# Kernel optimization log

Measured on AMD Instinct MI355X. Metric: run time of the kernel, lower is better.

## Reference

```python
import jax, jax.numpy as jnp
import numpy as np

EPS = 1e-15

def gcn_sparse(x, row, col, ew, W, b, n):
    # PyG GCNConv: h = x@W; add self-loops (weight 1); sym-normalize; aggregate at col (target); + bias
    h = x @ W
    loop = jnp.arange(n)
    r = jnp.concatenate([row, loop])
    c = jnp.concatenate([col, loop])
    w = jnp.concatenate([ew, jnp.ones((n,), x.dtype)])
    deg = jax.ops.segment_sum(w, c, num_segments=n)
    dinv = jnp.where(deg > 0, deg ** -0.5, 0.0)
    norm = dinv[r] * w * dinv[c]
    out = jax.ops.segment_sum(norm[:, None] * h[r], c, num_segments=n)
    return out + b

def gcn_dense(x, adj, W, b):
    # Dense equivalent of dense_to_sparse + GCNConv: existing nonzero self-loops keep their
    # weight, zero-diagonal nodes get a self-loop of weight 1 (add_remaining_self_loops).
    diag = jnp.diagonal(adj)
    adj_h = adj + jnp.diag(jnp.where(diag == 0, 1.0, 0.0).astype(adj.dtype))
    deg = adj_h.sum(axis=0)  # degree at target (col) nodes
    dinv = jnp.where(deg > 0, deg ** -0.5, 0.0)
    a_norm = dinv[:, None] * adj_h * dinv[None, :]  # norm_ij = d_i^-1/2 a_ij d_j^-1/2
    return a_norm.T @ (x @ W) + b  # out_j = sum_i norm_ij h_i

def diff_pool(x, adj, s, mask=None):
    s = jax.nn.softmax(s, axis=-1)
    if mask is not None:
        x = x * mask[:, None]
        s = s * mask[:, None]
    out = s.T @ x                      # [C, F]
    out_adj = s.T @ (adj @ s)          # [C, C]
    link = jnp.linalg.norm(adj - s @ s.T) / adj.size
    ent = jnp.mean(jnp.sum(-s * jnp.log(s + EPS), axis=-1))
    return out, out_adj, link, ent

def setup_inputs() -> dict:
    N, E, F, H, C1, C2, NC = 8192, 262144, 128, 128, 1024, 128, 16
    key = jax.random.key(0)
    ks = jax.random.split(key, 16)
    x0 = jax.random.normal(ks[0], (N, F), dtype=jnp.float32)
    edge_index = jax.random.randint(ks[1], (2, E), 0, N, dtype=jnp.int32)
    edge_weight = jax.random.uniform(ks[2], (E,), dtype=jnp.float32)
    adj = jnp.zeros((N, N), jnp.float32).at[edge_index[0], edge_index[1]].add(edge_weight)
    mask = jnp.ones((N,), jnp.float32)
    g = lambda k, i, o: jax.random.normal(k, (i, o), dtype=jnp.float32) * (1.0 / np.sqrt(i))
    return {
        'x0': x0, 'edge_index': edge_index, 'edge_weight': edge_weight,
        'adj': adj, 'mask': mask,
        'W0_in': g(ks[3], F, H),      'b0_in': jnp.zeros((H,)),
        'Wp1':   g(ks[4], H, C1),     'bp1':   jnp.zeros((C1,)),
        'W1_in': g(ks[5], H, H),      'b1_in': jnp.zeros((H,)),
        'Wp2':   g(ks[6], H, C2),     'bp2':   jnp.zeros((C2,)),
        'W2_in': g(ks[7], H, H),      'b2_in': jnp.zeros((H,)),
        'W1_out': g(ks[8], 2 * H, H), 'b1_out': jnp.zeros((H,)),
        'W0_out': g(ks[9], 2 * H, NC), 'b0_out': jnp.zeros((NC,)),
    }

def reference(x0, edge_index, edge_weight, adj, mask,
              W0_in, b0_in, Wp1, bp1, W1_in, b1_in, Wp2, bp2,
              W2_in, b2_in, W1_out, b1_out, W0_out, b0_out):
    n = x0.shape[0]
    row, col = edge_index[0], edge_index[1]
    x0_ = jax.nn.relu(gcn_sparse(x0, row, col, edge_weight, W0_in, b0_in, n))
    s1 = jax.nn.relu(gcn_sparse(x0_, row, col, edge_weight, Wp1, bp1, n))
    x1, adj1, l1, e1 = diff_pool(x0_, adj, s1, mask)
    x1_ = jax.nn.relu(gcn_dense(x1, adj1, W1_in, b1_in))
    s2 = jax.nn.relu(gcn_dense(x1_, adj1, Wp2, bp2))
    x2, adj2, l2, e2 = diff_pool(x1_, adj1, s2)
    x2_out = jax.nn.relu(gcn_dense(x2, adj2, W2_in, b2_in))
    x2_out_up = s2 @ x2_out  # unpool with pre-softmax relu s2, as in source
    x1_out = jax.nn.relu(gcn_dense(jnp.concatenate([x1_, x2_out_up], axis=1), adj1, W1_out, b1_out))
    x1_out_up = s1 @ x1_out
    x0_out = jax.nn.relu(gcn_sparse(jnp.concatenate([x0_, x1_out_up], axis=1), row, col, edge_weight, W0_out, b0_out, n))
    prediction = jax.nn.log_softmax(x0_out, axis=1)
    edge_loss = l1 + e1 + l2 + e2
    return prediction, s1, edge_loss, adj1
```

## Files before the change

### kernel.cpp

```cpp
#include <hip/hip_runtime.h>
#include <math.h>


#define N_NODES 8192
#define N_EDGES 262144

typedef __attribute__((ext_vector_type(8))) short short8;
typedef __attribute__((ext_vector_type(4))) float floatx4;

#define OFF_DEG     0
#define OFF_CNTC    8192
#define OFF_CNTR    16384
#define OFF_SCAL    24576
#define ZERO_FLOATS 24592
#define OFF_COLPTR  24592
#define OFF_ROWPTR  32785
#define OFF_CURC    40978
#define OFF_CURR    49170
#define OFF_COLR    57362
#define OFF_COLN    319506
#define OFF_ROWC    581650
#define OFF_ROWW    843794
#define OFF_DINV    1105938
#define OFF_X0      1114144
#define OFF_H0      2162720
#define OFF_S       3211296
#define OFF_AN1TB   OFF_S
#define OFF_ADJ1B   (OFF_S+524288)
#define OFF_HAT     (OFF_S+1048576)
#define OFF_HBT     (OFF_S+1114112)
#define OFF_HCATT   (OFF_S+1179648)
#define OFF_S2ST    (OFF_S+1245184)
#define OFF_X0T     7405600
#define OFF_X0B     7929888
#define A2          8454176
#define OFF_X1      (A2+0)
#define OFF_Y16     (A2+131072)
#define OFF_X1_     (A2+262144)
#define OFF_S2      (A2+524288)
#define OFF_S2S     (A2+655360)
#define OFF_U       (A2+786432)
#define OFF_X2      (A2+917504)
#define OFF_ADJ2    (A2+933888)
#define OFF_HC      (A2+950272)
#define OFF_X2_     (A2+966656)
#define OFF_AN2     (A2+983040)
#define OFF_Z2      (A2+999424)
#define OFF_HCAT    (A2+1130496)
#define OFF_X1O     (A2+1261568)
#define OFF_P16     (A2+1392640)
#define OFF_DI1     (A2+1654784)
#define OFF_DF1     (A2+1655808)
#define OFF_DI2     (A2+1656832)
#define OFF_DF2     (A2+1656960)
#define OFF_ST      10111264
#define OFF_TBF     14305568
#define OFF_WP1T    OFF_TBF
#define OFF_PADJ    OFF_TBF
#define OFF_PG      22694176
#define OFF_PP      OFF_PG
#define OFF_PX1     31082784
#define OFF_TT2     32131360

#define OUT_PRED 0
#define OUT_S1   131072
#define OUT_LOSS 8519680
#define OUT_ADJ1 8519681

__device__ __forceinline__ unsigned short f2bf(float f) {
    union { float f; unsigned u; } v; v.f = f;
    unsigned r = (v.u + 0x7FFF + ((v.u >> 16) & 1)) >> 16;
    return (unsigned short)r;
}
__device__ __forceinline__ float bf2f(unsigned short b) {
    union { unsigned u; float f; } v; v.u = (unsigned)b << 16; return v.f;
}


__global__ void k_hist(const int* __restrict__ row, const int* __restrict__ col,
                       const float* __restrict__ ew, int E,
                       float* deg, int* cntc, int* cntr, float* sumA2) {
    __shared__ float red[256];
    int e = blockIdx.x * 256 + threadIdx.x;
    float w2 = 0.f;
    if (e < E) {
        int r = row[e], c = col[e];
        float w = ew[e];
        atomicAdd(&deg[c], w);
        atomicAdd(&cntc[c], 1);
        atomicAdd(&cntr[r], 1);
        w2 = w * w;
    }
    red[threadIdx.x] = w2; __syncthreads();
    for (int s = 128; s > 0; s >>= 1) { if (threadIdx.x < s) red[threadIdx.x] += red[threadIdx.x + s]; __syncthreads(); }
    if (threadIdx.x == 0) atomicAdd(sumA2, red[0]);
}

__global__ __launch_bounds__(1024) void k_scan(const int* cntc, const int* cntr,
        int* colptr, int* rowptr, int* curc, int* curr, int n, int E,
        const float* __restrict__ deg, float* __restrict__ dinv) {
    __shared__ int part[1024];
    int tid = threadIdx.x;
    const int per = 8;
    for (int pass = 0; pass < 2; ++pass) {
        const int* cnt = pass ? cntr : cntc;
        int* ptr = pass ? rowptr : colptr;
        int* cur = pass ? curr : curc;
        int st = tid * per;
// ... 117 lines not shown
    for (int k0 = 0; k0 < K; k0 += 32) {
        #pragma unroll
        for (int l = 0; l < 4; ++l) {
            int idx = tid + 256 * l;
            int r = idx >> 5, c = idx & 31;
            As[r][c] = A[(size_t)(m0 + r) * K + k0 + c];
            Bs[r][c] = B[(size_t)(k0 + r) * N + n0 + c];
        }
        __syncthreads();
        #pragma unroll
        for (int kk = 0; kk < 32; ++kk) {
            float a0 = As[ty * 2][kk], a1 = As[ty * 2 + 1][kk];
            float b0 = Bs[kk][tx * 2], b1 = Bs[kk][tx * 2 + 1];
            acc[0][0] += a0 * b0; acc[0][1] += a0 * b1;
            acc[1][0] += a1 * b0; acc[1][1] += a1 * b1;
        }
        __syncthreads();
    }
    #pragma unroll
    for (int i = 0; i < 2; ++i)
        #pragma unroll
        for (int j = 0; j < 2; ++j)
            As[ty * 2 + i][tx * 2 + j] = acc[i][j];
    __syncthreads();
    int nl = tid >> 3, moff = (tid & 7) * 4;
    ushort4 o;
    o.x = f2bf(As[moff + 0][nl]);
    o.y = f2bf(As[moff + 1][nl]);
    o.z = f2bf(As[moff + 2][nl]);
    o.w = f2bf(As[moff + 3][nl]);
    *(ushort4*)(CT + (size_t)(n0 + nl) * M + m0 + moff) = o;
}

__global__ __launch_bounds__(256) void gemm_atb32(const float* __restrict__ A, const float* __restrict__ B,
        float* __restrict__ C, int M, int N, int K,
        const float* __restrict__ bias, int relu, float* sumsq_acc) {
    __shared__ float As[32][33];
    __shared__ float Bs[32][33];
    __shared__ float red[256];
    int tid = threadIdx.x, tx = tid & 15, ty = tid >> 4;
    int m0 = blockIdx.y * 32, n0 = blockIdx.x * 32;
    float acc[2][2] = {};
    for (int k0 = 0; k0 < K; k0 += 32) {
        #pragma unroll
        for (int l = 0; l < 4; ++l) {
            int idx = tid + 256 * l;
            int r = idx >> 5, c = idx & 31;
            As[c][r] = A[(size_t)(k0 + r) * M + m0 + c];
            Bs[r][c] = B[(size_t)(k0 + r) * N + n0 + c];
        }
        __syncthreads();
        #pragma unroll
        for (int kk = 0; kk < 32; ++kk) {
            float a0 = As[ty * 2][kk], a1 = As[ty * 2 + 1][kk];
            float b0 = Bs[kk][tx * 2], b1 = Bs[kk][tx * 2 + 1];
            acc[0][0] += a0 * b0; acc[0][1] += a0 * b1;
            acc[1][0] += a1 * b0; acc[1][1] += a1 * b1;
        }
        __syncthreads();
    }
    if (sumsq_acc) {
        float ss = acc[0][0] * acc[0][0] + acc[0][1] * acc[0][1]
                 + acc[1][0] * acc[1][0] + acc[1][1] * acc[1][1];
        red[tid] = ss; __syncthreads();
        for (int s = 128; s > 0; s >>= 1) { if (tid < s) red[tid] += red[tid + s]; __syncthreads(); }
        if (tid == 0) atomicAdd(sumsq_acc, red[0]);
        return;
    }
    #pragma unroll
    for (int i = 0; i < 2; ++i)
        #pragma unroll
        for (int j = 0; j < 2; ++j) {
            int m = m0 + ty * 2 + i, n = n0 + tx * 2 + j;
            float v = acc[i][j];
            if (bias) v += bias[n];
            if (relu) v = fmaxf(v, 0.f);
            C[(size_t)m * N + n] = v;
        }
}

__global__ __launch_bounds__(256) void k_atb32_3(const float* __restrict__ A,
        const float* __restrict__ B0, const float* __restrict__ B1, const float* __restrict__ B2,
        float* __restrict__ C0, float* __restrict__ C1, float* ss_acc,
        int M, int N, int K) {
    __shared__ float As[32][33];
    __shared__ float Bs[32][33];
    __shared__ float red[256];
    int op = blockIdx.z;
    const float* B = (op == 0) ? B0 : (op == 1) ? B1 : B2;
    int tid = threadIdx.x, tx = tid & 15, ty = tid >> 4;
    int m0 = blockIdx.y * 32, n0 = blockIdx.x * 32;
    float acc[2][2] = {};
    for (int k0 = 0; k0 < K; k0 += 32) {
        #pragma unroll
        for (int l = 0; l < 4; ++l) {
            int idx = tid + 256 * l;
            int r = idx >> 5, c = idx & 31;
            As[c][r] = A[(size_t)(k0 + r) * M + m0 + c];
            Bs[r][c] = B[(size_t)(k0 + r) * N + n0 + c];
        }
        __syncthreads();
        #pragma unroll
        for (int kk = 0; kk < 32; ++kk) {
            float a0 = As[ty * 2][kk], a1 = As[ty * 2 + 1][kk];
            float b0 = Bs[kk][tx * 2], b1 = Bs[kk][tx * 2 + 1];
            acc[0][0] += a0 * b0; acc[0][1] += a0 * b1;
            acc[1][0] += a1 * b0; acc[1][1] += a1 * b1;
        }
        __syncthreads();
    }
// ... 10 lines not shown
    for (int i = 0; i < 2; ++i)
        #pragma unroll
        for (int j = 0; j < 2; ++j)
            C[(size_t)(m0 + ty * 2 + i) * N + n0 + tx * 2 + j] = acc[i][j];
}

__global__ __launch_bounds__(256) void k_gemm_n16(const float* __restrict__ A, const float* __restrict__ B,
        float* __restrict__ C, int M, int K, int accum) {
    __shared__ float As[16][64];
    __shared__ float Bs[64][16];
    int tid = threadIdx.x;
    int r = tid >> 4, c = tid & 15;
    int m0 = blockIdx.x * 16;
    float acc = 0.f;
    for (int k0 = 0; k0 < K; k0 += 64) {
        #pragma unroll
        for (int l = 0; l < 4; ++l) {
            int idx = tid + 256 * l;
            int rr = idx >> 6, cc = idx & 63;
            As[rr][cc] = A[(size_t)(m0 + rr) * K + k0 + cc];
            int kk = idx >> 4, c2 = idx & 15;
            Bs[kk][c2] = B[(size_t)(k0 + kk) * 16 + c2];
        }
        __syncthreads();
        #pragma unroll 16
        for (int kk = 0; kk < 64; ++kk) acc += As[r][kk] * Bs[kk][c];
        __syncthreads();
    }
    float* p = &C[(size_t)(m0 + r) * 16 + c];
    if (accum) acc += *p;
    *p = acc;
}


__global__ __launch_bounds__(256) void gemm_tn_bf16_part(
        const unsigned short* __restrict__ A, const unsigned short* __restrict__ B,
        float* __restrict__ P, int M, int N, int K) {
    __shared__ __align__(16) unsigned short As[128 * 64];
    __shared__ __align__(16) unsigned short Bs[128 * 64];
    int tid = threadIdx.x;
    int wave = tid >> 6, lane = tid & 63;
    int wm = wave >> 1, wn = wave & 1;
    int m0 = blockIdx.x * 128, n0 = blockIdx.y * 128;
    int kchunk = K / gridDim.z;
    int k0 = blockIdx.z * kchunk;
    float* Pz = P + (size_t)blockIdx.z * M * N;
    floatx4 acc[4][4] = {};
    int sr = tid >> 3;
    int sc = (tid & 7) * 8;
    int q = lane >> 4, lm = lane & 15;
    for (int kt = 0; kt < kchunk; kt += 64) {
        #pragma unroll
        for (int p = 0; p < 4; ++p) {
            int mrow = sr + p * 32;
            int gk = k0 + kt + sc;
            int scs = sc ^ ((mrow & 7) * 8);
            *(short8*)(&As[mrow * 64 + scs]) = *(const short8*)(&A[(size_t)(m0 + mrow) * K + gk]);
            *(short8*)(&Bs[mrow * 64 + scs]) = *(const short8*)(&B[(size_t)(n0 + mrow) * K + gk]);
        }
        __syncthreads();
        #pragma unroll
        for (int ks = 0; ks < 64; ks += 32) {
            short8 af[4], bf[4];
            int kk = ks + q * 8;
            #pragma unroll
            for (int i = 0; i < 4; ++i) {
                int ml = wm * 64 + i * 16 + lm;
                af[i] = *(const short8*)(&As[ml * 64 + (kk ^ ((ml & 7) * 8))]);
                int nl = wn * 64 + i * 16 + lm;
                bf[i] = *(const short8*)(&Bs[nl * 64 + (kk ^ ((nl & 7) * 8))]);
            }
            #pragma unroll
            for (int i = 0; i < 4; ++i)
                #pragma unroll
                for (int j = 0; j < 4; ++j)
                    acc[i][j] = __builtin_amdgcn_mfma_f32_16x16x32_bf16(af[i], bf[j], acc[i][j], 0, 0, 0);
        }
        __syncthreads();
    }
    for (int i = 0; i < 4; ++i) {
        int rowb = m0 + wm * 64 + i * 16 + q * 4;
        for (int j = 0; j < 4; ++j) {
            int col = n0 + wn * 64 + j * 16 + lm;
            #pragma unroll
            for (int r = 0; r < 4; ++r)
                Pz[(size_t)(rowb + r) * N + col] = acc[i][j][r];
        }
    }
}

__global__ __launch_bounds__(256) void gemm_tn_bf16_part3(
        const unsigned short* __restrict__ A,
        const unsigned short* __restrict__ B0, const unsigned short* __restrict__ B1,
        const unsigned short* __restrict__ B2,
        float* __restrict__ P0, float* __restrict__ P1, float* __restrict__ P2,
        int K) {
    __shared__ __align__(16) unsigned short As[128 * 64];
    __shared__ __align__(16) unsigned short Bs[128 * 64];
    int tid = threadIdx.x;
    int wave = tid >> 6, lane = tid & 63;
    int wm = wave >> 1, wn = wave & 1;
    int by = blockIdx.y;
    const unsigned short* B; float* P; int N, n0;
    if (by < 8)       { B = B0; P = P0; N = 1024; n0 = by * 128; }
    else if (by < 16) { B = B1; P = P1; N = 1024; n0 = (by - 8) * 128; }
    else              { B = B2; P = P2; N = 128;  n0 = 0; }
    int m0 = blockIdx.x * 128;
    int kchunk = K / gridDim.z;
    int k0 = blockIdx.z * kchunk;
    float* Pz = P + (size_t)blockIdx.z * 1024 * N;
    floatx4 acc[4][4] = {};
    int sr = tid >> 3;
    int sc = (tid & 7) * 8;
    int q = lane >> 4, lm = lane & 15;
    for (int kt = 0; kt < kchunk; kt += 64) {
        #pragma unroll
        for (int p = 0; p < 4; ++p) {
            int mrow = sr + p * 32;
            int gk = k0 + kt + sc;
            int scs = sc ^ ((mrow & 7) * 8);
            *(short8*)(&As[mrow * 64 + scs]) = *(const short8*)(&A[(size_t)(m0 + mrow) * K + gk]);
            *(short8*)(&Bs[mrow * 64 + scs]) = *(const short8*)(&B[(size_t)(n0 + mrow) * K + gk]);
        }
        __syncthreads();
        #pragma unroll
        for (int ks = 0; ks < 64; ks += 32) {
            short8 af[4], bf[4];
            int kk = ks + q * 8;
            #pragma unroll
            for (int i = 0; i < 4; ++i) {
                int ml = wm * 64 + i * 16 + lm;
                af[i] = *(const short8*)(&As[ml * 64 + (kk ^ ((ml & 7) * 8))]);
                int nl = wn * 64 + i * 16 + lm;
                bf[i] = *(const short8*)(&Bs[nl * 64 + (kk ^ ((nl & 7) * 8))]);
            }
            #pragma unroll
            for (int i = 0; i < 4; ++i)
                #pragma unroll
                for (int j = 0; j < 4; ++j)
                    acc[i][j] = __builtin_amdgcn_mfma_f32_16x16x32_bf16(af[i], bf[j], acc[i][j], 0, 0, 0);
        }
        __syncthreads();
    }
    for (int i = 0; i < 4; ++i) {
        int rowb = m0 + wm * 64 + i * 16 + q * 4;
        for (int j = 0; j < 4; ++j) {
            int col = n0 + wn * 64 + j * 16 + lm;
            #pragma unroll
            for (int r = 0; r < 4; ++r)
                Pz[(size_t)(rowb + r) * N + col] = acc[i][j][r];
        }
    }
}

__global__ __launch_bounds__(256) void gemm_tn_bf16_store(
        const unsigned short* __restrict__ A, const unsigned short* __restrict__ B,
        float* __restrict__ C, int M, int N, int K,
        const float* __restrict__ bias, int relu) {
    __shared__ __align__(16) unsigned short As[128 * 64];
    __shared__ __align__(16) unsigned short Bs[128 * 64];
    int tid = threadIdx.x;
    int wave = tid >> 6, lane = tid & 63;
    int wm = wave >> 1, wn = wave & 1;
    int m0 = blockIdx.x * 128, n0 = blockIdx.y * 128;
    floatx4 acc[4][4] = {};
    int sr = tid >> 3;
    int sc = (tid & 7) * 8;
    int q = lane >> 4, lm = lane & 15;
    for (int kt = 0; kt < K; kt += 64) {
        #pragma unroll
        for (int p = 0; p < 4; ++p) {
            int mrow = sr + p * 32;
            int gk = kt + sc;
            int scs = sc ^ ((mrow & 7) * 8);
            *(short8*)(&As[mrow * 64 + scs]) = *(const short8*)(&A[(size_t)(m0 + mrow) * K + gk]);
            *(short8*)(&Bs[mrow * 64 + scs]) = *(const short8*)(&B[(size_t)(n0 + mrow) * K + gk]);
        }
        __syncthreads();
        #pragma unroll
        for (int ks = 0; ks < 64; ks += 32) {
            short8 af[4], bf[4];
            int kk = ks + q * 8;
            #pragma unroll
            for (int i = 0; i < 4; ++i) {
                int ml = wm * 64 + i * 16 + lm;
                af[i] = *(const short8*)(&As[ml * 64 + (kk ^ ((ml & 7) * 8))]);
                int nl = wn * 64 + i * 16 + lm;
                bf[i] = *(const short8*)(&Bs[nl * 64 + (kk ^ ((nl & 7) * 8))]);
            }
            #pragma unroll
            for (int i = 0; i < 4; ++i)
                #pragma unroll
                for (int j = 0; j < 4; ++j)
                    acc[i][j] = __builtin_amdgcn_mfma_f32_16x16x32_bf16(af[i], bf[j], acc[i][j], 0, 0, 0);
        }
        __syncthreads();
    }
    for (int i = 0; i < 4; ++i) {
        int rowb = m0 + wm * 64 + i * 16 + q * 4;
        for (int j = 0; j < 4; ++j) {
            int col = n0 + wn * 64 + j * 16 + lm;
            float bv = bias ? bias[col] : 0.f;
            #pragma unroll
            for (int r = 0; r < 4; ++r) {
                float v = acc[i][j][r] + bv;
                if (relu) v = fmaxf(v, 0.f);
                C[(size_t)(rowb + r) * N + col] = v;
            }
        }
    }
}

__global__ __launch_bounds__(256) void k_reduce4(const float* __restrict__ P,
        float* __restrict__ C, unsigned short* __restrict__ Cb,
        int n, int nsplit, float* ss_acc) {
    __shared__ float red[256];
    float ss = 0.f;
    for (int i4 = (blockIdx.x * 256 + threadIdx.x) * 4; i4 < n; i4 += gridDim.x * 256 * 4) {
        float4 v = *(const float4*)(P + i4);
        for (int s = 1; s < nsplit; ++s) {
            float4 w = *(const float4*)(P + (size_t)s * n + i4);
            v.x += w.x; v.y += w.y; v.z += w.z; v.w += w.w;
        }
        if (C) *(float4*)(C + i4) = v;
        if (Cb) {
            ushort4 o; o.x = f2bf(v.x); o.y = f2bf(v.y); o.z = f2bf(v.z); o.w = f2bf(v.w);
            *(ushort4*)(Cb + i4) = o;
        }
        ss += v.x * v.x + v.y * v.y + v.z * v.z + v.w * v.w;
    }
    if (!ss_acc) return;
    red[threadIdx.x] = ss; __syncthreads();
    for (int s = 128; s > 0; s >>= 1) { if (threadIdx.x < s) red[threadIdx.x] += red[threadIdx.x + s]; __syncthreads(); }
    if (threadIdx.x == 0) atomicAdd(ss_acc, red[0]);
}

__global__ __launch_bounds__(256) void k_reduce_br(const float* __restrict__ P,
        float* __restrict__ C, int n, int N, int nsplit,
        const float* __restrict__ bias, int relu) {
    for (int i4 = (blockIdx.x * 256 + threadIdx.x) * 4; i4 < n; i4 += gridDim.x * 256 * 4) {
        float4 v = *(const float4*)(P + i4);
        for (int s = 1; s < nsplit; ++s) {
            float4 w = *(const float4*)(P + (size_t)s * n + i4);
            v.x += w.x; v.y += w.y; v.z += w.z; v.w += w.w;
        }
        if (bias) {
            float4 b = *(const float4*)(bias + (i4 % N));
            v.x += b.x; v.y += b.y; v.z += b.z; v.w += b.w;
        }
        if (relu) {
            v.x = fmaxf(v.x, 0.f); v.y = fmaxf(v.y, 0.f);
            v.z = fmaxf(v.z, 0.f); v.w = fmaxf(v.w, 0.f);
        }
        *(float4*)(C + i4) = v;
    }
}


__global__ __launch_bounds__(256) void k_transpose_f2b(
        const float* __restrict__ in, unsigned short* __restrict__ outb,
        int R, int C, const float* __restrict__ rowscale) {
    __shared__ float tile[64][65];
    int rb = blockIdx.y * 64, cb = blockIdx.x * 64;
    int t = threadIdx.x;
    int lr = t >> 4, lc4 = (t & 15) * 4;
    #pragma unroll
    for (int p = 0; p < 4; ++p) {
// ... 179 lines not shown
__global__ __launch_bounds__(256) void k_softmax_ent(const float* __restrict__ x, float* __restrict__ S,
        int W, const float* __restrict__ mask, float* ent_acc) {
    __shared__ float red[256];
    int row = blockIdx.x, tid = threadIdx.x;
    const float* xr = x + (size_t)row * W;
    float m = -3.0e38f;
    for (int q = tid; q < W; q += 256) m = fmaxf(m, xr[q]);
    red[tid] = m; __syncthreads();
    for (int s = 128; s > 0; s >>= 1) { if (tid < s) red[tid] = fmaxf(red[tid], red[tid + s]); __syncthreads(); }
    m = red[0]; __syncthreads();
    float sum = 0.f;
    for (int q = tid; q < W; q += 256) sum += expf(xr[q] - m);
    red[tid] = sum; __syncthreads();
    for (int s = 128; s > 0; s >>= 1) { if (tid < s) red[tid] += red[tid + s]; __syncthreads(); }
    float inv = 1.0f / red[0]; __syncthreads();
    float mk = mask ? mask[row] : 1.0f;
    float* Sr = S + (size_t)row * W;
    float ent = 0.f;
    for (int q = tid; q < W; q += 256) {
        float v = expf(xr[q] - m) * inv * mk;
        Sr[q] = v;
        ent -= v * logf(v + 1e-15f);
    }
    red[tid] = ent; __syncthreads();
    for (int s = 128; s > 0; s >>= 1) { if (tid < s) red[tid] += red[tid + s]; __syncthreads(); }
    if (tid == 0) atomicAdd(ent_acc, red[0]);
}

__global__ __launch_bounds__(256) void k_spmm_seg(const unsigned short* __restrict__ Sb,
        const int* __restrict__ rptr, const int* __restrict__ rowc, const float* __restrict__ roww,
        unsigned short* __restrict__ tb) {
    int wave = threadIdx.x >> 6, lane = threadIdx.x & 63;
    int r = blockIdx.x * 4 + wave;
    int j0 = blockIdx.y * 128 + lane * 2;
    const unsigned short* Sj = Sb + j0;
    float a0 = 0.f, a1 = 0.f;
    int e0 = rptr[r], e1 = rptr[r + 1];
    int e = e0;
    for (; e + 4 <= e1; e += 4) {
        int c0 = rowc[e], c1 = rowc[e + 1], c2 = rowc[e + 2], c3 = rowc[e + 3];
        float w0 = roww[e], w1 = roww[e + 1], w2 = roww[e + 2], w3 = roww[e + 3];
        unsigned v0 = *(const unsigned*)(Sj + (size_t)c0 * 1024);
        unsigned v1 = *(const unsigned*)(Sj + (size_t)c1 * 1024);
        unsigned v2 = *(const unsigned*)(Sj + (size_t)c2 * 1024);
        unsigned v3 = *(const unsigned*)(Sj + (size_t)c3 * 1024);
        a0 += w0 * bf2f((unsigned short)(v0 & 0xffff)) + w1 * bf2f((unsigned short)(v1 & 0xffff))
            + w2 * bf2f((unsigned short)(v2 & 0xffff)) + w3 * bf2f((unsigned short)(v3 & 0xffff));
        a1 += w0 * bf2f((unsigned short)(v0 >> 16)) + w1 * bf2f((unsigned short)(v1 >> 16))
            + w2 * bf2f((unsigned short)(v2 >> 16)) + w3 * bf2f((unsigned short)(v3 >> 16));
    }
    for (; e < e1; ++e) {
        int c = rowc[e]; float w = roww[e];
        unsigned v = *(const unsigned*)(Sj + (size_t)c * 1024);
        a0 += w * bf2f((unsigned short)(v & 0xffff));
        a1 += w * bf2f((unsigned short)(v >> 16));
    }
    unsigned o = (unsigned)f2bf(a0) | ((unsigned)f2bf(a1) << 16);
    *(unsigned*)(tb + (size_t)r * 1024 + j0) = o;
}

__global__ void k_colsum_part(const float* __restrict__ adjm, int n, float* part) {
    int j = blockIdx.x * blockDim.x + threadIdx.x;
    if (j >= n) return;
    int r0 = blockIdx.y * 64;
    float s = 0.f;
    for (int r = r0; r < r0 + 64; ++r) s += adjm[(size_t)r * n + j];
    part[(size_t)blockIdx.y * n + j] = s;
}

__global__ void k_dfix_part(const float* __restrict__ adjm, int n, const float* __restrict__ part,
                            int nparts, float* dinvv, float* dfix, float* cross_acc) {
    __shared__ float red[256];
    int j = blockIdx.x * blockDim.x + threadIdx.x;
    float diag = 0.f;
    if (j < n) {
        float s = 0.f;
        for (int p = 0; p < nparts; ++p) s += part[(size_t)p * n + j];
        diag = adjm[(size_t)j * n + j];
        float fix = (diag == 0.f) ? 1.0f : 0.f;
        s += fix;
        dfix[j] = fix;
        dinvv[j] = (s > 0.f) ? 1.0f / sqrtf(s) : 0.f;
    }
    red[threadIdx.x] = diag; __syncthreads();
    for (int s = 128; s > 0; s >>= 1) { if (threadIdx.x < s) red[threadIdx.x] += red[threadIdx.x + s]; __syncthreads(); }
    if (threadIdx.x == 0) atomicAdd(cross_acc, red[0]);
}

__global__ __launch_bounds__(128) void k_coldfix128(const float* __restrict__ adjm,
        float* dinvv, float* dfix, float* cross2_out) {
    __shared__ float red[128];
    int j = threadIdx.x;
    float s = 0.f;
    for (int i = 0; i < 128; ++i) s += adjm[(size_t)i * 128 + j];
    float diag = adjm[(size_t)j * 128 + j];
    float fix = (diag == 0.f) ? 1.0f : 0.f;
    s += fix;
    dfix[j] = fix;
    dinvv[j] = (s > 0.f) ? 1.0f / sqrtf(s) : 0.f;
    red[j] = diag; __syncthreads();
    for (int st = 64; st > 0; st >>= 1) { if (j < st) red[j] += red[j + st]; __syncthreads(); }
    if (j == 0) *cross2_out = red[0];
}

__global__ void k_anorm(const float* __restrict__ adjm, int n, const float* __restrict__ dinvv,
                        const float* __restrict__ dfix, float* __restrict__ anorm) {
    int idx = blockIdx.x * 256 + threadIdx.x;
    if (idx >= n * n) return;
    int i = idx / n, j = idx % n;
    float v = adjm[idx] + ((i == j) ? dfix[j] : 0.f);
    anorm[idx] = dinvv[i] * v * dinvv[j];
}

__global__ void k_finalize(const float* __restrict__ sc, float* loss) {
    if (threadIdx.x == 0 && blockIdx.x == 0) {
        float e1     = sc[0] / 8192.0f;
        float cross  = sc[1];
        float g2     = sc[2];
        float sumA2  = sc[3];
        float ssadj1 = sc[4];
        float e2     = sc[5] / 1024.0f;
        float cross2 = sc[6];
        float g2b    = sc[7];
        float l1 = sqrtf(fmaxf(sumA2 - 2.0f * cross + g2, 0.f)) / 67108864.0f;
        float l2 = sqrtf(fmaxf(ssadj1 - 2.0f * cross2 + g2b, 0.f)) / 1048576.0f;
        *loss = l1 + e1 + l2 + e2;
    }
}


extern "C" void kernel_launch(void* const* d_in, const int* in_sizes, int n_in,
                              void* d_out, int out_size, void* d_ws, size_t ws_size,
                              hipStream_t stream) {
    const int N = N_NODES, E = N_EDGES;
    const float* x0     = (const float*)d_in[0];
    const int*   eidx   = (const int*)d_in[1];
    const float* ew     = (const float*)d_in[2];
    const float* mask   = (const float*)d_in[4];
    const float* W0_in  = (const float*)d_in[5];
    const float* b0_in  = (const float*)d_in[6];
    const float* Wp1    = (const float*)d_in[7];
    const float* bp1    = (const float*)d_in[8];
    const float* W1_in  = (const float*)d_in[9];
    const float* b1_in  = (const float*)d_in[10];
// ... 26 lines not shown
    float* coln  = wsf + OFF_COLN;
    int*   rowc  = wsi + OFF_ROWC;
    float* roww  = wsf + OFF_ROWW;
    float* dinv  = wsf + OFF_DINV;
    float* x0_   = wsf + OFF_X0;
    unsigned short* h0b   = (unsigned short*)(wsf + OFF_H0);
    unsigned short* Sb    = (unsigned short*)(wsf + OFF_S);
    unsigned short* TT    = (unsigned short*)(wsf + OFF_TT2);
    unsigned short* AN1TB = (unsigned short*)(wsf + OFF_AN1TB);
    unsigned short* ADJ1B = (unsigned short*)(wsf + OFF_ADJ1B);
    unsigned short* HAT   = (unsigned short*)(wsf + OFF_HAT);
    unsigned short* HBT   = (unsigned short*)(wsf + OFF_HBT);
    unsigned short* HCATT = (unsigned short*)(wsf + OFF_HCATT);
    unsigned short* S2ST  = (unsigned short*)(wsf + OFF_S2ST);
    unsigned short* ST    = (unsigned short*)(wsf + OFF_ST);
    unsigned short* TBF   = (unsigned short*)(wsf + OFF_TBF);
    unsigned short* WP1T  = (unsigned short*)(wsf + OFF_WP1T);
    unsigned short* X0T   = (unsigned short*)(wsf + OFF_X0T);
    unsigned short* x0b   = (unsigned short*)(wsf + OFF_X0B);
    float* PADJ  = wsf + OFF_PADJ;
    float* PG    = wsf + OFF_PG;
    float* PP    = wsf + OFF_PP;
    float* PX1   = wsf + OFF_PX1;
    float* x1    = wsf + OFF_X1;
    float* y16   = wsf + OFF_Y16;
    float* x1_   = wsf + OFF_X1_;
    float* s2    = wsf + OFF_S2;
    float* S2s   = wsf + OFF_S2S;
    float* u     = wsf + OFF_U;
    float* x2    = wsf + OFF_X2;
    float* adj2  = wsf + OFF_ADJ2;
    float* hC    = wsf + OFF_HC;
    float* x2_   = wsf + OFF_X2_;
    float* an2   = wsf + OFF_AN2;
    float* z2    = wsf + OFF_Z2;
    float* hcat  = wsf + OFF_HCAT;
    float* x1o_  = wsf + OFF_X1O;
    float* p16   = wsf + OFF_P16;
    float* di1   = wsf + OFF_DI1;
    float* df1   = wsf + OFF_DF1;
    float* di2   = wsf + OFF_DI2;
    float* df2   = wsf + OFF_DF2;
    float* cspart = wsf + OFF_CURC;

    const int* row = eidx;
    const int* col = eidx + E;

    hipMemsetAsync(wsf, 0, (size_t)ZERO_FLOATS * sizeof(float), stream);

    k_hist<<<E / 256, 256, 0, stream>>>(row, col, ew, E, deg, cntc, cntr, &scal[3]);
    k_scan<<<1, 1024, 0, stream>>>(cntc, cntr, cptr, rptr, curc, curr, N, E, deg, dinv);
    k_scatter<<<E / 256, 256, 0, stream>>>(row, col, ew, E, dinv, curc, curr, colr, coln, rowc, roww);

    gemm_ab_b16<<<dim3(2, 128), 256, 0, stream>>>(x0, W0_in, h0b, 8192, 128, 128);
    k_agg_b16<<<N, 64, 0, stream>>>(h0b, x0_, x0b, cptr, colr, coln, dinv, b0_in, 1);

    k_agg_b16<<<N, 64, 0, stream>>>(x0b, nullptr, h0b, cptr, colr, coln, dinv, nullptr, 0);
    k_transpose_f2b<<<dim3(16, 2), 256, 0, stream>>>(Wp1, WP1T, 128, 1024, nullptr);
    gemm_tn_bf16_store<<<dim3(64, 8), 256, 0, stream>>>(h0b, WP1T, s1o, 8192, 1024, 128, bp1, 1);

    k_softmax1024<<<N, 256, 0, stream>>>(s1o, Sb, mask, &scal[0]);
    k_spmm_seg<<<dim3(N / 4, 8), 256, 0, stream>>>(Sb, rptr, rowc, roww, TBF);
    k_transpose_b2b2<<<dim3(16, 128, 2), 256, 0, stream>>>(Sb, ST, TBF, TT, 8192, 1024);
    k_transpose_f2b<<<dim3(2, 128), 256, 0, stream>>>(x0_, X0T, 8192, 128, mask);

    gemm_tn_bf16_part3<<<dim3(8, 17, 8), 256, 0, stream>>>(ST, TT, ST, X0T, PADJ, PG, PX1, 8192);
    k_reduce4<<<1024, 256, 0, stream>>>(PADJ, adj1o, ADJ1B, 1024 * 1024, 8, &scal[4]);
    k_reduce4<<<1024, 256, 0, stream>>>(PG, nullptr, nullptr, 1024 * 1024, 8, &scal[2]);
    k_reduce4<<<128, 256, 0, stream>>>(PX1, x1, nullptr, 1024 * 128, 8, nullptr);

    k_colsum_part<<<dim3(4, 16), 256, 0, stream>>>(adj1o, 1024, cspart);
    k_dfix_part<<<4, 256, 0, stream>>>(adj1o, 1024, cspart, 16, di1, df1, &scal[1]);
    k_anorm_tb<<<dim3(16, 16), 256, 0, stream>>>(adj1o, 1024, di1, df1, AN1TB);

    gemm_ab32_bt<<<dim3(4, 32), 256, 0, stream>>>(x1, W1_in, HAT, 1024, 128, 128);
    gemm_tn_bf16_part<<<dim3(8, 1, 16), 256, 0, stream>>>(AN1TB, HAT, PP, 1024, 128, 1024);
    k_reduce_br<<<128, 256, 0, stream>>>(PP, x1_, 1024 * 128, 128, 16, b1_in, 1);
    gemm_ab32_bt<<<dim3(4, 32), 256, 0, stream>>>(x1_, Wp2, HBT, 1024, 128, 128);
    gemm_tn_bf16_part<<<dim3(8, 1, 16), 256, 0, stream>>>(AN1TB, HBT, PP, 1024, 128, 1024);
    k_reduce_br<<<128, 256, 0, stream>>>(PP, s2, 1024 * 128, 128, 16, bp2, 1);

    k_softmax_ent<<<1024, 256, 0, stream>>>(s2, S2s, 128, nullptr, &scal[5]);
    k_transpose_f2b<<<dim3(2, 16), 256, 0, stream>>>(S2s, S2ST, 1024, 128, nullptr);
    gemm_tn_bf16_part<<<dim3(8, 1, 16), 256, 0, stream>>>(ADJ1B, S2ST, PP, 1024, 128, 1024);
    k_reduce_br<<<128, 256, 0, stream>>>(PP, u, 1024 * 128, 128, 16, nullptr, 0);
    k_atb32_3<<<dim3(4, 4, 3), 256, 0, stream>>>(S2s, x1_, u, S2s, x2, adj2, &scal[7], 128, 128, 1024);

    k_coldfix128<<<1, 128, 0, stream>>>(adj2, di2, df2, &scal[6]);
    k_anorm<<<64, 256, 0, stream>>>(adj2, 128, di2, df2, an2);
    gemm_ab32<<<dim3(4, 4), 256, 0, stream>>>(x2, W2_in, hC, 128, 128, 128, nullptr, 0, 0);
    gemm_atb32<<<dim3(4, 4), 256, 0, stream>>>(an2, hC, x2_, 128, 128, 128, b2_in, 1, nullptr);

    gemm_ab32<<<dim3(4, 4), 256, 0, stream>>>(x2_, W1_out + 128 * 128, z2, 128, 128, 128, nullptr, 0, 0);
    gemm_ab32<<<dim3(4, 32), 256, 0, stream>>>(x1_, W1_out, hcat, 1024, 128, 128, nullptr, 0, 0);
    gemm_ab32<<<dim3(4, 32), 256, 0, stream>>>(s2, z2, hcat, 1024, 128, 128, nullptr, 0, 1);
    k_transpose_f2b<<<dim3(2, 16), 256, 0, stream>>>(hcat, HCATT, 1024, 128, nullptr);
    gemm_tn_bf16_part<<<dim3(8, 1, 16), 256, 0, stream>>>(AN1TB, HCATT, PP, 1024, 128, 1024);
    k_reduce_br<<<128, 256, 0, stream>>>(PP, x1o_, 1024 * 128, 128, 16, b1_out, 1);

    k_gemm_n16<<<64, 256, 0, stream>>>(x1o_, W0_out + 128 * 16, y16, 1024, 128, 0);
    k_gemm_n16<<<512, 256, 0, stream>>>(x0_, W0_out, p16, 8192, 128, 0);
    k_gemm_n16<<<512, 256, 0, stream>>>(s1o, y16, p16, 8192, 1024, 1);
    k_agg16_ls<<<512, 256, 0, stream>>>(p16, predo, cptr, colr, coln, dinv, b0_out);

    k_finalize<<<1, 64, 0, stream>>>(scal, losso);
}
```

Measured before the change: 967.4 us.

## Fuse small kernels, use direct global-to-LDS loads in bf16 GEMMs, widen spmm

Several launch pairs are merged into single kernels: the three partial-sum reductions, the column-sum and degree-fix passes, the normalized-adjacency build folded into the 128x128 GEMM, the two-source concat GEMMs plus transpose, and the two n16 GEMMs. The bf16 MFMA GEMMs now stage tiles with global_load_lds instead of going through registers. The segment spmm processes four columns per lane instead of two. The aim is fewer launches and intermediate buffers and cheaper tile staging, at the cost of more complex kernels and reliance on the swizzle staying correct under the new LDS write pattern.

```diff
diff --git a/kernel.cpp b/kernel.cpp
--- a/kernel.cpp
+++ b/kernel.cpp
@@ -44,9 +44,7 @@
 #define OFF_ADJ2    (A2+933888)
 #define OFF_HC      (A2+950272)
 #define OFF_X2_     (A2+966656)
-#define OFF_AN2     (A2+983040)
 #define OFF_Z2      (A2+999424)
-#define OFF_HCAT    (A2+1130496)
 #define OFF_X1O     (A2+1261568)
 #define OFF_P16     (A2+1392640)
 #define OFF_DI1     (A2+1654784)
@@ -74,6 +72,11 @@
 }
 __device__ __forceinline__ float bf2f(unsigned short b) {
     union { unsigned u; float f; } v; v.u = (unsigned)b << 16; return v.f;
+}
+__device__ __forceinline__ void gl_lds16(const unsigned short* g, unsigned short* l) {
+    __builtin_amdgcn_global_load_lds(
+        (const __attribute__((address_space(1))) void*)g,
+        (__attribute__((address_space(3))) void*)l, 16, 0, 0);
 }
 
 
@@ -257,12 +260,57 @@
     *(ushort4*)(CT + (size_t)(n0 + nl) * M + m0 + moff) = o;
 }
 
-__global__ __launch_bounds__(256) void gemm_atb32(const float* __restrict__ A, const float* __restrict__ B,
-        float* __restrict__ C, int M, int N, int K,
-        const float* __restrict__ bias, int relu, float* sumsq_acc) {
+__global__ __launch_bounds__(256) void gemm_dual_bt(const float* __restrict__ A0,
+        const float* __restrict__ B0, const float* __restrict__ A1, const float* __restrict__ B1,
+        unsigned short* __restrict__ CT, int M, int N, int Kc) {
     __shared__ float As[32][33];
     __shared__ float Bs[32][33];
-    __shared__ float red[256];
+    int tid = threadIdx.x, tx = tid & 15, ty = tid >> 4;
+    int m0 = blockIdx.y * 32, n0 = blockIdx.x * 32;
+    float acc[2][2] = {};
+    for (int src = 0; src < 2; ++src) {
+        const float* A = src ? A1 : A0;
+        const float* B = src ? B1 : B0;
+        for (int k0 = 0; k0 < Kc; k0 += 32) {
+            #pragma unroll
+            for (int l = 0; l < 4; ++l) {
+                int idx = tid + 256 * l;
+                int r = idx >> 5, c = idx & 31;
+                As[r][c] = A[(size_t)(m0 + r) * Kc + k0 + c];
+                Bs[r][c] = B[(size_t)(k0 + r) * N + n0 + c];
+            }
+            __syncthreads();
+            #pragma unroll
+            for (int kk = 0; kk < 32; ++kk) {
+                float a0 = As[ty * 2][kk], a1 = As[ty * 2 + 1][kk];
+                float b0 = Bs[kk][tx * 2], b1 = Bs[kk][tx * 2 + 1];
+                acc[0][0] += a0 * b0; acc[0][1] += a0 * b1;
+                acc[1][0] += a1 * b0; acc[1][1] += a1 * b1;
+            }
+            __syncthreads();
+        }
+    }
+    #pragma unroll
+    for (int i = 0; i < 2; ++i)
+        #pragma unroll
+        for (int j = 0; j < 2; ++j)
+            As[ty * 2 + i][tx * 2 + j] = acc[i][j];
+    __syncthreads();
+    int nl = tid >> 3, moff = (tid & 7) * 4;
+    ushort4 o;
+    o.x = f2bf(As[moff + 0][nl]);
+    o.y = f2bf(As[moff + 1][nl]);
+    o.z = f2bf(As[moff + 2][nl]);
+    o.w = f2bf(As[moff + 3][nl]);
+    *(ushort4*)(CT + (size_t)(n0 + nl) * M + m0 + moff) = o;
+}
+
+__global__ __launch_bounds__(256) void gemm_atb32n(const float* __restrict__ A, const float* __restrict__ B,
+        float* __restrict__ C, int M, int N, int K,
+        const float* __restrict__ bias, const float* __restrict__ kscale,
+        const float* __restrict__ dfixv, const float* __restrict__ mscale) {
+    __shared__ float As[32][33];
+    __shared__ float Bs[32][33];
     int tid = threadIdx.x, tx = tid & 15, ty = tid >> 4;
     int m0 = blockIdx.y * 32, n0 = blockIdx.x * 32;
     float acc[2][2] = {};
@@ -271,8 +319,11 @@
         for (int l = 0; l < 4; ++l) {
             int idx = tid + 256 * l;
             int r = idx >> 5, c = idx & 31;
-            As[c][r] = A[(size_t)(k0 + r) * M + m0 + c];
-            Bs[r][c] = B[(size_t)(k0 + r) * N + n0 + c];
+            int k = k0 + r, m = m0 + c;
+            float v = A[(size_t)k * M + m];
+            if (k == m) v += dfixv[m];
+            As[c][r] = v * kscale[k];
+            Bs[r][c] = B[(size_t)k * N + n0 + c];
         }
         __syncthreads();
         #pragma unroll
@@ -284,23 +335,13 @@
         }
         __syncthreads();
     }
-    if (sumsq_acc) {
-        float ss = acc[0][0] * acc[0][0] + acc[0][1] * acc[0][1]
-                 + acc[1][0] * acc[1][0] + acc[1][1] * acc[1][1];
-        red[tid] = ss; __syncthreads();
-        for (int s = 128; s > 0; s >>= 1) { if (tid < s) red[tid] += red[tid + s]; __syncthreads(); }
-        if (tid == 0) atomicAdd(sumsq_acc, red[0]);
-        return;
-    }
     #pragma unroll
     for (int i = 0; i < 2; ++i)
         #pragma unroll
         for (int j = 0; j < 2; ++j) {
             int m = m0 + ty * 2 + i, n = n0 + tx * 2 + j;
-            float v = acc[i][j];
-            if (bias) v += bias[n];
-            if (relu) v = fmaxf(v, 0.f);
-            C[(size_t)m * N + n] = v;
+            float v = acc[i][j] * mscale[m] + bias[n];
+            C[(size_t)m * N + n] = fmaxf(v, 0.f);
         }
 }
 
@@ -377,6 +418,38 @@
     *p = acc;
 }
 
+__global__ __launch_bounds__(256) void k_gemm_n16_dual(
+        const float* __restrict__ A0, int K0, const float* __restrict__ B0,
+        const float* __restrict__ A1, int K1, const float* __restrict__ B1,
+        float* __restrict__ C, int M) {
+    __shared__ float As[16][64];
+    __shared__ float Bs[64][16];
+    int tid = threadIdx.x;
+    int r = tid >> 4, c = tid & 15;
+    int m0 = blockIdx.x * 16;
+    float acc = 0.f;
+    for (int src = 0; src < 2; ++src) {
+        const float* A = src ? A1 : A0;
+        const float* B = src ? B1 : B0;
+        int K = src ? K1 : K0;
+        for (int k0 = 0; k0 < K; k0 += 64) {
+            #pragma unroll
+            for (int l = 0; l < 4; ++l) {
+                int idx = tid + 256 * l;
+                int rr = idx >> 6, cc = idx & 63;
+                As[rr][cc] = A[(size_t)(m0 + rr) * K + k0 + cc];
+                int kk = idx >> 4, c2 = idx & 15;
+                Bs[kk][c2] = B[(size_t)(k0 + kk) * 16 + c2];
+            }
+            __syncthreads();
+            #pragma unroll 16
+            for (int kk = 0; kk < 64; ++kk) acc += As[r][kk] * Bs[kk][c];
+            __syncthreads();
+        }
+    }
+    C[(size_t)(m0 + r) * 16 + c] = acc;
+}
+
 
 __global__ __launch_bounds__(256) void gemm_tn_bf16_part(
         const unsigned short* __restrict__ A, const unsigned short* __restrict__ B,
@@ -391,17 +464,17 @@
     int k0 = blockIdx.z * kchunk;
     float* Pz = P + (size_t)blockIdx.z * M * N;
     floatx4 acc[4][4] = {};
-    int sr = tid >> 3;
-    int sc = (tid & 7) * 8;
     int q = lane >> 4, lm = lane & 15;
+    int lrow = lane >> 3, lcol = (lane & 7) * 8;
     for (int kt = 0; kt < kchunk; kt += 64) {
+        int gk0 = k0 + kt;
         #pragma unroll
         for (int p = 0; p < 4; ++p) {
-            int mrow = sr + p * 32;
-            int gk = k0 + kt + sc;
-            int scs = sc ^ ((mrow & 7) * 8);
-            *(short8*)(&As[mrow * 64 + scs]) = *(const short8*)(&A[(size_t)(m0 + mrow) * K + gk]);
-            *(short8*)(&Bs[mrow * 64 + scs]) = *(const short8*)(&B[(size_t)(n0 + mrow) * K + gk]);
+            int rbase = wave * 32 + p * 8;
+            int row = rbase + lrow;
+            int scol = lcol ^ ((row & 7) * 8);
+            gl_lds16(&A[(size_t)(m0 + row) * K + gk0 + scol], &As[rbase * 64]);
+            gl_lds16(&B[(size_t)(n0 + row) * K + gk0 + scol], &Bs[rbase * 64]);
         }
         __syncthreads();
         #pragma unroll
@@ -455,17 +528,17 @@
     int k0 = blockIdx.z * kchunk;
     float* Pz = P + (size_t)blockIdx.z * 1024 * N;
     floatx4 acc[4][4] = {};
-    int sr = tid >> 3;
-    int sc = (tid & 7) * 8;
     int q = lane >> 4, lm = lane & 15;
+    int lrow = lane >> 3, lcol = (lane & 7) * 8;
     for (int kt = 0; kt < kchunk; kt += 64) {
+        int gk0 = k0 + kt;
         #pragma unroll
         for (int p = 0; p < 4; ++p) {
-            int mrow = sr + p * 32;
-            int gk = k0 + kt + sc;
-            int scs = sc ^ ((mrow & 7) * 8);
-            *(short8*)(&As[mrow * 64 + scs]) = *(const short8*)(&A[(size_t)(m0 + mrow) * K + gk]);
-            *(short8*)(&Bs[mrow * 64 + scs]) = *(const short8*)(&B[(size_t)(n0 + mrow) * K + gk]);
+            int rbase = wave * 32 + p * 8;
+            int row = rbase + lrow;
+            int scol = lcol ^ ((row & 7) * 8);
+            gl_lds16(&A[(size_t)(m0 + row) * K + gk0 + scol], &As[rbase * 64]);
+            gl_lds16(&B[(size_t)(n0 + row) * K + gk0 + scol], &Bs[rbase * 64]);
         }
         __syncthreads();
         #pragma unroll
@@ -509,17 +582,16 @@
     int wm = wave >> 1, wn = wave & 1;
     int m0 = blockIdx.x * 128, n0 = blockIdx.y * 128;
     floatx4 acc[4][4] = {};
-    int sr = tid >> 3;
-    int sc = (tid & 7) * 8;
     int q = lane >> 4, lm = lane & 15;
+    int lrow = lane >> 3, lcol = (lane & 7) * 8;
     for (int kt = 0; kt < K; kt += 64) {
         #pragma unroll
         for (int p = 0; p < 4; ++p) {
-            int mrow = sr + p * 32;
-            int gk = kt + sc;
-            int scs = sc ^ ((mrow & 7) * 8);
-            *(short8*)(&As[mrow * 64 + scs]) = *(const short8*)(&A[(size_t)(m0 + mrow) * K + gk]);
-            *(short8*)(&Bs[mrow * 64 + scs]) = *(const short8*)(&B[(size_t)(n0 + mrow) * K + gk]);
+            int rbase = wave * 32 + p * 8;
+            int row = rbase + lrow;
+            int scol = lcol ^ ((row & 7) * 8);
+            gl_lds16(&A[(size_t)(m0 + row) * K + kt + scol], &As[rbase * 64]);
+            gl_lds16(&B[(size_t)(n0 + row) * K + kt + scol], &Bs[rbase * 64]);
         }
         __syncthreads();
         #pragma unroll
@@ -556,14 +628,20 @@
     }
 }
 
-__global__ __launch_bounds__(256) void k_reduce4(const float* __restrict__ P,
-        float* __restrict__ C, unsigned short* __restrict__ Cb,
-        int n, int nsplit, float* ss_acc) {
+__global__ __launch_bounds__(256) void k_reduce3m(
+        const float* __restrict__ P0, float* __restrict__ C0, unsigned short* __restrict__ Cb0, float* ss0,
+        const float* __restrict__ P1, float* ss1,
+        const float* __restrict__ P2, float* __restrict__ C2) {
     __shared__ float red[256];
-    float ss = 0.f;
+    const float* P; float* C; unsigned short* Cb; float* ss; int n;
+    if (blockIdx.y == 0)      { P = P0; C = C0;      Cb = Cb0;     ss = ss0;     n = 1024 * 1024; }
+    else if (blockIdx.y == 1) { P = P1; C = nullptr; Cb = nullptr; ss = ss1;     n = 1024 * 1024; }
+    else                      { P = P2; C = C2;      Cb = nullptr; ss = nullptr; n = 1024 * 128; }
+    float ssv = 0.f;
     for (int i4 = (blockIdx.x * 256 + threadIdx.x) * 4; i4 < n; i4 += gridDim.x * 256 * 4) {
         float4 v = *(const float4*)(P + i4);
-        for (int s = 1; s < nsplit; ++s) {
+        #pragma unroll
+        for (int s = 1; s < 8; ++s) {
             float4 w = *(const float4*)(P + (size_t)s * n + i4);
             v.x += w.x; v.y += w.y; v.z += w.z; v.w += w.w;
         }
@@ -572,12 +650,12 @@
             ushort4 o; o.x = f2bf(v.x); o.y = f2bf(v.y); o.z = f2bf(v.z); o.w = f2bf(v.w);
             *(ushort4*)(Cb + i4) = o;
         }
-        ss += v.x * v.x + v.y * v.y + v.z * v.z + v.w * v.w;
-    }
-    if (!ss_acc) return;
-    red[threadIdx.x] = ss; __syncthreads();
+        ssv += v.x * v.x + v.y * v.y + v.z * v.z + v.w * v.w;
+    }
+    if (!ss) return;
+    red[threadIdx.x] = ssv; __syncthreads();
     for (int s = 128; s > 0; s >>= 1) { if (threadIdx.x < s) red[threadIdx.x] += red[threadIdx.x + s]; __syncthreads(); }
-    if (threadIdx.x == 0) atomicAdd(ss_acc, red[0]);
+    if (threadIdx.x == 0) atomicAdd(ss, red[0]);
 }
 
 __global__ __launch_bounds__(256) void k_reduce_br(const float* __restrict__ P,
@@ -823,58 +901,64 @@
         unsigned short* __restrict__ tb) {
     int wave = threadIdx.x >> 6, lane = threadIdx.x & 63;
     int r = blockIdx.x * 4 + wave;
-    int j0 = blockIdx.y * 128 + lane * 2;
+    int j0 = blockIdx.y * 256 + lane * 4;
     const unsigned short* Sj = Sb + j0;
-    float a0 = 0.f, a1 = 0.f;
+    float a0 = 0.f, a1 = 0.f, a2 = 0.f, a3 = 0.f;
     int e0 = rptr[r], e1 = rptr[r + 1];
     int e = e0;
     for (; e + 4 <= e1; e += 4) {
         int c0 = rowc[e], c1 = rowc[e + 1], c2 = rowc[e + 2], c3 = rowc[e + 3];
         float w0 = roww[e], w1 = roww[e + 1], w2 = roww[e + 2], w3 = roww[e + 3];
-        unsigned v0 = *(const unsigned*)(Sj + (size_t)c0 * 1024);
-        unsigned v1 = *(const unsigned*)(Sj + (size_t)c1 * 1024);
-        unsigned v2 = *(const unsigned*)(Sj + (size_t)c2 * 1024);
-        unsigned v3 = *(const unsigned*)(Sj + (size_t)c3 * 1024);
-        a0 += w0 * bf2f((unsigned short)(v0 & 0xffff)) + w1 * bf2f((unsigned short)(v1 & 0xffff))
-            + w2 * bf2f((unsigned short)(v2 & 0xffff)) + w3 * bf2f((unsigned short)(v3 & 0xffff));
-        a1 += w0 * bf2f((unsigned short)(v0 >> 16)) + w1 * bf2f((unsigned short)(v1 >> 16))
-            + w2 * bf2f((unsigned short)(v2 >> 16)) + w3 * bf2f((unsigned short)(v3 >> 16));
+        uint2 v0 = *(const uint2*)(Sj + (size_t)c0 * 1024);
+        uint2 v1 = *(const uint2*)(Sj + (size_t)c1 * 1024);
+        uint2 v2 = *(const uint2*)(Sj + (size_t)c2 * 1024);
+        uint2 v3 = *(const uint2*)(Sj + (size_t)c3 * 1024);
+        a0 += w0 * bf2f((unsigned short)(v0.x & 0xffff)) + w1 * bf2f((unsigned short)(v1.x & 0xffff))
+            + w2 * bf2f((unsigned short)(v2.x & 0xffff)) + w3 * bf2f((unsigned short)(v3.x & 0xffff));
+        a1 += w0 * bf2f((unsigned short)(v0.x >> 16)) + w1 * bf2f((unsigned short)(v1.x >> 16))
+            + w2 * bf2f((unsigned short)(v2.x >> 16)) + w3 * bf2f((unsigned short)(v3.x >> 16));
+        a2 += w0 * bf2f((unsigned short)(v0.y & 0xffff)) + w1 * bf2f((unsigned short)(v1.y & 0xffff))
+            + w2 * bf2f((unsigned short)(v2.y & 0xffff)) + w3 * bf2f((unsigned short)(v3.y & 0xffff));
+        a3 += w0 * bf2f((unsigned short)(v0.y >> 16)) + w1 * bf2f((unsigned short)(v1.y >> 16))
+            + w2 * bf2f((unsigned short)(v2.y >> 16)) + w3 * bf2f((unsigned short)(v3.y >> 16));
     }
     for (; e < e1; ++e) {
         int c = rowc[e]; float w = roww[e];
-        unsigned v = *(const unsigned*)(Sj + (size_t)c * 1024);
-        a0 += w * bf2f((unsigned short)(v & 0xffff));
-        a1 += w * bf2f((unsigned short)(v >> 16));
-    }
-    unsigned o = (unsigned)f2bf(a0) | ((unsigned)f2bf(a1) << 16);
-    *(unsigned*)(tb + (size_t)r * 1024 + j0) = o;
-}
-
-__global__ void k_colsum_part(const float* __restrict__ adjm, int n, float* part) {
-    int j = blockIdx.x * blockDim.x + threadIdx.x;
-    if (j >= n) return;
-    int r0 = blockIdx.y * 64;
+        uint2 v = *(const uint2*)(Sj + (size_t)c * 1024);
+        a0 += w * bf2f((unsigned short)(v.x & 0xffff));
+        a1 += w * bf2f((unsigned short)(v.x >> 16));
+        a2 += w * bf2f((unsigned short)(v.y & 0xffff));
+        a3 += w * bf2f((unsigned short)(v.y >> 16));
+    }
+    unsigned lo = (unsigned)f2bf(a0) | ((unsigned)f2bf(a1) << 16);
+    unsigned hi = (unsigned)f2bf(a2) | ((unsigned)f2bf(a3) << 16);
+    unsigned long long o = (unsigned long long)lo | ((unsigned long long)hi << 32);
+    *(unsigned long long*)(tb + (size_t)r * 1024 + j0) = o;
+}
+
+__global__ __launch_bounds__(256) void k_coldfix1024(const float* __restrict__ adjm,
+        float* dinvv, float* dfix, float* cross_acc) {
+    __shared__ float part[4][64];
+    __shared__ float red[256];
+    int jl = threadIdx.x & 63;
+    int j = blockIdx.x * 64 + jl;
+    int rg = threadIdx.x >> 6;
     float s = 0.f;
-    for (int r = r0; r < r0 + 64; ++r) s += adjm[(size_t)r * n + j];
-    part[(size_t)blockIdx.y * n + j] = s;
-}
-
-__global__ void k_dfix_part(const float* __restrict__ adjm, int n, const float* __restrict__ part,
-                            int nparts, float* dinvv, float* dfix, float* cross_acc) {
-    __shared__ float red[256];
-    int j = blockIdx.x * blockDim.x + threadIdx.x;
+    for (int r = rg * 256; r < rg * 256 + 256; ++r)
+        s += adjm[(size_t)r * 1024 + j];
+    part[rg][jl] = s;
+    __syncthreads();
     float diag = 0.f;
-    if (j < n) {
-        float s = 0.f;
-        for (int p = 0; p < nparts; ++p) s += part[(size_t)p * n + j];
-        diag = adjm[(size_t)j * n + j];
+    if (rg == 0) {
+        float tot = part[0][jl] + part[1][jl] + part[2][jl] + part[3][jl];
+        diag = adjm[(size_t)j * 1024 + j];
         float fix = (diag == 0.f) ? 1.0f : 0.f;
-        s += fix;
+        tot += fix;
         dfix[j] = fix;
-        dinvv[j] = (s > 0.f) ? 1.0f / sqrtf(s) : 0.f;
+        dinvv[j] = (tot > 0.f) ? 1.0f / sqrtf(tot) : 0.f;
     }
     red[threadIdx.x] = diag; __syncthreads();
-    for (int s = 128; s > 0; s >>= 1) { if (threadIdx.x < s) red[threadIdx.x] += red[threadIdx.x + s]; __syncthreads(); }
+    for (int st = 128; st > 0; st >>= 1) { if (threadIdx.x < st) red[threadIdx.x] += red[threadIdx.x + st]; __syncthreads(); }
     if (threadIdx.x == 0) atomicAdd(cross_acc, red[0]);
 }
 
@@ -892,15 +976,6 @@
     red[j] = diag; __syncthreads();
     for (int st = 64; st > 0; st >>= 1) { if (j < st) red[j] += red[j + st]; __syncthreads(); }
     if (j == 0) *cross2_out = red[0];
-}
-
-__global__ void k_anorm(const float* __restrict__ adjm, int n, const float* __restrict__ dinvv,
-                        const float* __restrict__ dfix, float* __restrict__ anorm) {
-    int idx = blockIdx.x * 256 + threadIdx.x;
-    if (idx >= n * n) return;
-    int i = idx / n, j = idx % n;
-    float v = adjm[idx] + ((i == j) ? dfix[j] : 0.f);
-    anorm[idx] = dinvv[i] * v * dinvv[j];
 }
 
 __global__ void k_finalize(const float* __restrict__ sc, float* loss) {
@@ -993,16 +1068,13 @@
     float* adj2  = wsf + OFF_ADJ2;
     float* hC    = wsf + OFF_HC;
     float* x2_   = wsf + OFF_X2_;
-    float* an2   = wsf + OFF_AN2;
     float* z2    = wsf + OFF_Z2;
-    float* hcat  = wsf + OFF_HCAT;
     float* x1o_  = wsf + OFF_X1O;
     float* p16   = wsf + OFF_P16;
     float* di1   = wsf + OFF_DI1;
     float* df1   = wsf + OFF_DF1;
     float* di2   = wsf + OFF_DI2;
     float* df2   = wsf + OFF_DF2;
-    float* cspart = wsf + OFF_CURC;
 
     const int* row = eidx;
     const int* col = eidx + E;
@@ -1021,17 +1093,14 @@
     gemm_tn_bf16_store<<<dim3(64, 8), 256, 0, stream>>>(h0b, WP1T, s1o, 8192, 1024, 128, bp1, 1);
 
     k_softmax1024<<<N, 256, 0, stream>>>(s1o, Sb, mask, &scal[0]);
-    k_spmm_seg<<<dim3(N / 4, 8), 256, 0, stream>>>(Sb, rptr, rowc, roww, TBF);
+    k_spmm_seg<<<dim3(N / 4, 4), 256, 0, stream>>>(Sb, rptr, rowc, roww, TBF);
     k_transpose_b2b2<<<dim3(16, 128, 2), 256, 0, stream>>>(Sb, ST, TBF, TT, 8192, 1024);
     k_transpose_f2b<<<dim3(2, 128), 256, 0, stream>>>(x0_, X0T, 8192, 128, mask);
 
     gemm_tn_bf16_part3<<<dim3(8, 17, 8), 256, 0, stream>>>(ST, TT, ST, X0T, PADJ, PG, PX1, 8192);
-    k_reduce4<<<1024, 256, 0, stream>>>(PADJ, adj1o, ADJ1B, 1024 * 1024, 8, &scal[4]);
-    k_reduce4<<<1024, 256, 0, stream>>>(PG, nullptr, nullptr, 1024 * 1024, 8, &scal[2]);
-    k_reduce4<<<128, 256, 0, stream>>>(PX1, x1, nullptr, 1024 * 128, 8, nullptr);
-
-    k_colsum_part<<<dim3(4, 16), 256, 0, stream>>>(adj1o, 1024, cspart);
-    k_dfix_part<<<4, 256, 0, stream>>>(adj1o, 1024, cspart, 16, di1, df1, &scal[1]);
+    k_reduce3m<<<dim3(1024, 3), 256, 0, stream>>>(PADJ, adj1o, ADJ1B, &scal[4], PG, &scal[2], PX1, x1);
+
+    k_coldfix1024<<<16, 256, 0, stream>>>(adj1o, di1, df1, &scal[1]);
     k_anorm_tb<<<dim3(16, 16), 256, 0, stream>>>(adj1o, 1024, di1, df1, AN1TB);
 
     gemm_ab32_bt<<<dim3(4, 32), 256, 0, stream>>>(x1, W1_in, HAT, 1024, 128, 128);
@@ -1048,20 +1117,16 @@
     k_atb32_3<<<dim3(4, 4, 3), 256, 0, stream>>>(S2s, x1_, u, S2s, x2, adj2, &scal[7], 128, 128, 1024);
 
     k_coldfix128<<<1, 128, 0, stream>>>(adj2, di2, df2, &scal[6]);
-    k_anorm<<<64, 256, 0, stream>>>(adj2, 128, di2, df2, an2);
     gemm_ab32<<<dim3(4, 4), 256, 0, stream>>>(x2, W2_in, hC, 128, 128, 128, nullptr, 0, 0);
-    gemm_atb32<<<dim3(4, 4), 256, 0, stream>>>(an2, hC, x2_, 128, 128, 128, b2_in, 1, nullptr);
+    gemm_atb32n<<<dim3(4, 4), 256, 0, stream>>>(adj2, hC, x2_, 128, 128, 128, b2_in, di2, df2, di2);
 
     gemm_ab32<<<dim3(4, 4), 256, 0, stream>>>(x2_, W1_out + 128 * 128, z2, 128, 128, 128, nullptr, 0, 0);
-    gemm_ab32<<<dim3(4, 32), 256, 0, stream>>>(x1_, W1_out, hcat, 1024, 128, 128, nullptr, 0, 0);
-    gemm_ab32<<<dim3(4, 32), 256, 0, stream>>>(s2, z2, hcat, 1024, 128, 128, nullptr, 0, 1);
-    k_transpose_f2b<<<dim3(2, 16), 256, 0, stream>>>(hcat, HCATT, 1024, 128, nullptr);
+    gemm_dual_bt<<<dim3(4, 32), 256, 0, stream>>>(x1_, W1_out, s2, z2, HCATT, 1024, 128, 128);
     gemm_tn_bf16_part<<<dim3(8, 1, 16), 256, 0, stream>>>(AN1TB, HCATT, PP, 1024, 128, 1024);
     k_reduce_br<<<128, 256, 0, stream>>>(PP, x1o_, 1024 * 128, 128, 16, b1_out, 1);
 
     k_gemm_n16<<<64, 256, 0, stream>>>(x1o_, W0_out + 128 * 16, y16, 1024, 128, 0);
-    k_gemm_n16<<<512, 256, 0, stream>>>(x0_, W0_out, p16, 8192, 128, 0);
-    k_gemm_n16<<<512, 256, 0, stream>>>(s1o, y16, p16, 8192, 1024, 1);
+    k_gemm_n16_dual<<<512, 256, 0, stream>>>(x0_, 128, W0_out, s1o, 1024, y16, p16, 8192);
     k_agg16_ls<<<512, 256, 0, stream>>>(p16, predo, cptr, colr, coln, dinv, b0_out);
 
     k_finalize<<<1, 64, 0, stream>>>(scal, losso);
```

Result: faster. 945.8 us (-2.2%).
